# Kernel tuning notes

Hardware: AMD Instinct MI355X
Metric: run time of the kernel (lower is better)

## Reference

```python
import jax, jax.numpy as jnp
import numpy as np

B, C, H, W = 2, 256, 64, 64
NUM_HEADS = 8


def setup_inputs() -> dict:
    key = jax.random.key(0)
    k1, k2, k3 = jax.random.split(key, 3)
    x = jax.random.normal(k1, (B, C, H, W), dtype=jnp.float32)
    # 1x1 convs, bias=False -> plain [out_ch, in_ch] matrices
    w_qkv = jax.random.normal(k2, (3 * C, C), dtype=jnp.float32) * (1.0 / np.sqrt(C))
    w_proj = jax.random.normal(k3, (C, C), dtype=jnp.float32) * (1.0 / np.sqrt(C))
    return {"x": x, "w_qkv": w_qkv, "w_proj": w_proj}


def reference(x, w_qkv, w_proj):
    b, c, h, w = x.shape
    hd = NUM_HEADS
    d = c // hd  # head dim
    n = h * w    # number of tokens

    # 1x1 conv == channel matmul: [3C, C] x [B, C, H, W] -> [B, 3C, H, W]
    qkv = jnp.einsum('oc,bchw->bohw', w_qkv, x)
    q, k, v = jnp.split(qkv, 3, axis=1)

    def reshape(t):
        return t.reshape(b, hd, d, n)  # [B, h, d, N]

    q, k, v = map(reshape, (q, k, v))

    # scores[b,h,i,j] = sum_d q[b,h,d,i] * k[b,h,d,j] / sqrt(d)
    scores = jnp.einsum('bhdi,bhdj->bhij', q, k) / jnp.sqrt(jnp.asarray(d, x.dtype))
    attn = jax.nn.softmax(scores, axis=-1)

    # out[b,h,d,i] = sum_j attn[b,h,i,j] * v[b,h,d,j]
    out = jnp.einsum('bhij,bhdj->bhdi', attn, v)
    out = out.reshape(b, c, h, w)

    return jnp.einsum('oc,bchw->bohw', w_proj, out) + x
```

## Files before the change

### kernel.cpp

```cpp
#include <hip/hip_runtime.h>
#include <hip/hip_bf16.h>

#define NB  2
#define CC  256
#define NHD 8
#define HD  32
#define NT  4096

typedef __bf16 bf16x8 __attribute__((ext_vector_type(8)));
typedef bf16x8 bf16x8_ma __attribute__((may_alias));
typedef __bf16 bf16x4 __attribute__((ext_vector_type(4)));
typedef bf16x4 bf16x4_ma __attribute__((may_alias));
typedef float  f32x4  __attribute__((ext_vector_type(4)));
typedef float  f32x16 __attribute__((ext_vector_type(16)));
typedef unsigned int u32x4 __attribute__((ext_vector_type(4)));

static __device__ __forceinline__ f32x4 zero4() {
    f32x4 z = {0.f, 0.f, 0.f, 0.f}; return z;
}
static __device__ __forceinline__ f32x16 zero16() {
    f32x16 z = {0.f,0.f,0.f,0.f,0.f,0.f,0.f,0.f,
                0.f,0.f,0.f,0.f,0.f,0.f,0.f,0.f};
    return z;
}

#define QSCALE 0.25505392421795654f

#define CVT_PK(dst, lo, hi_) \
    asm("v_cvt_pk_bf16_f32 %0, %1, %2" : "=v"(dst) : "v"(lo), "v"(hi_))
#define PLSWAP(x, y) \
    asm("v_permlane32_swap_b32 %0, %1" : "+v"(x), "+v"(y))


__global__ __launch_bounds__(256) void convw_k(const float* __restrict__ s1,
                                               __bf16* __restrict__ d1, int n1,
                                               const float* __restrict__ s2,
                                               __bf16* __restrict__ d2, int n2) {
    const int i = blockIdx.x * 256 + threadIdx.x;
    if (i < n1) d1[i] = (__bf16)s1[i];
    else if (i - n1 < n2) d2[i - n1] = (__bf16)s2[i - n1];
}

__global__ __launch_bounds__(256) void transpose_k(const float* __restrict__ x,
                                                   __bf16* __restrict__ xt) {
    __shared__ __bf16 T[64][65];
    const int tid = threadIdx.x;
    const int n0 = blockIdx.x * 64, c0 = blockIdx.y * 64, b = blockIdx.z;

#pragma unroll
    for (int rep = 0; rep < 16; ++rep) {
        const int e = rep * 256 + tid;
        const int cl = e >> 6, nl = e & 63;
        T[nl][cl] = (__bf16)x[((size_t)(b * CC + c0 + cl)) * NT + n0 + nl];
    }
    __syncthreads();
#pragma unroll
    for (int rep = 0; rep < 16; ++rep) {
        const int e = rep * 256 + tid;
        const int nl = e >> 6, cl = e & 63;
        xt[((size_t)(b * NT + n0 + nl)) * CC + c0 + cl] = T[nl][cl];
    }
}

__global__ __launch_bounds__(256) void qkv_k(const __bf16* __restrict__ wqkv,
                                             const __bf16* __restrict__ xt,
                                             __bf16* __restrict__ qt,
                                             __bf16* __restrict__ kt,
                                             __bf16* __restrict__ vv) {
    __shared__ __align__(16) __bf16 BF[4][8][512];

    const int lane = threadIdx.x & 63, wv = threadIdx.x >> 6;
    const int g = lane >> 4, c16 = lane & 15;
    const int b    = blockIdx.z;
    const int o0   = blockIdx.y * 64 + wv * 16;
    const int tok0 = blockIdx.x * 64;

    const __bf16* bsrc = xt + ((size_t)(b * NT + tok0 + wv * 16 + c16)) * CC + g * 8;
#pragma unroll
    for (int kc = 0; kc < 8; ++kc) {
        __builtin_amdgcn_global_load_lds(
            (const __attribute__((address_space(1))) void*)(bsrc + kc * 32),
            (__attribute__((address_space(3))) void*)&BF[wv][kc][0],
            16, 0, 0);
    }

    const __bf16* arow = wqkv + (size_t)(o0 + c16) * CC + g * 8;
    bf16x8 a[8];
#pragma unroll
    for (int kc = 0; kc < 8; ++kc) a[kc] = *(const bf16x8_ma*)(arow + kc * 32);

    __syncthreads();

    f32x4 acc[4];
#pragma unroll
    for (int i = 0; i < 4; ++i) acc[i] = zero4();

#pragma unroll
    for (int kc = 0; kc < 8; ++kc) {
#pragma unroll
        for (int js = 0; js < 4; ++js) {
            bf16x8 bb = *(const bf16x8_ma*)&BF[js][kc][lane * 8];
            acc[js] = __builtin_amdgcn_mfma_f32_16x16x32_bf16(a[kc], bb, acc[js], 0, 0, 0);
        }
    }

    const int reg = o0 >> 8;
    const int oo0 = (o0 & 255) + g * 4;
    const int h   = oo0 >> 5;
    const int dd0 = oo0 & 31;
    const size_t bh = (size_t)(b * NHD + h);

#pragma unroll
    for (int js = 0; js < 4; ++js) {
        const int tok = tok0 + js * 16 + c16;
        if (reg == 0) {
            bf16x4 pk;
#pragma unroll
            for (int r = 0; r < 4; ++r) pk[r] = (__bf16)(acc[js][r] * QSCALE);
            *(bf16x4_ma*)(qt + (bh * NT + tok) * HD + dd0) = pk;
        } else if (reg == 1) {
            bf16x4 pk;
#pragma unroll
            for (int r = 0; r < 4; ++r) pk[r] = (__bf16)acc[js][r];
            *(bf16x4_ma*)(kt + (bh * NT + tok) * HD + dd0) = pk;
        } else {
#pragma unroll
            for (int r = 0; r < 4; ++r)
                vv[(bh * HD + dd0 + r) * NT + tok] = (__bf16)acc[js][r];
        }
    }
}

__global__ __launch_bounds__(256, 2) void attn_k(const __bf16* __restrict__ qt,
                                                 const __bf16* __restrict__ kt,
                                                 const __bf16* __restrict__ vv,
                                                 __bf16* __restrict__ ao) {
    __shared__ __align__(16) __bf16 KF[4][2][2][512];
    __shared__ __align__(16) __bf16 VF[4][2][2][512];

    const int tid  = threadIdx.x;
    const int lane = tid & 63, wv = tid >> 6;
    const int c32 = lane & 31, hi = lane >> 5;
    const int bh = blockIdx.y;
    const int b = bh >> 3, h = bh & 7;
    const int i0q = blockIdx.x * 128 + wv * 32;

    const __bf16* qbase = qt + ((size_t)bh * NT + i0q) * HD;
    const __bf16* kbase = kt + (size_t)bh * NT * HD;
    const __bf16* vbase = vv + (size_t)bh * HD * NT;

    const int stg_js = wv & 1, stg_sl = wv >> 1;

    bf16x8 aq0 = *(const bf16x8_ma*)(qbase + (size_t)c32 * HD + hi * 8);
    bf16x8 aq1 = *(const bf16x8_ma*)(qbase + (size_t)c32 * HD + 16 + hi * 8);

    f32x16 oacc = zero16();
    float rsa[4] = {0.f, 0.f, 0.f, 0.f};

#define STAGE(bf, jb) do {                                                              \
    const __bf16* gk = kbase + (size_t)((jb) + stg_js * 32 + c32) * HD                  \
                             + stg_sl * 16 + hi * 8;                                    \
    __builtin_amdgcn_global_load_lds(                                                   \
        (const __attribute__((address_space(1))) void*)gk,                              \
        (__attribute__((address_space(3))) void*)&KF[bf][stg_js][stg_sl][0],            \
        16, 0, 0);                                                                      \
    const __bf16* gv = vbase + (size_t)c32 * NT + (jb) + stg_js * 32                    \
                             + stg_sl * 16 + hi * 8;                                    \
    __builtin_amdgcn_global_load_lds(                                                   \
        (const __attribute__((address_space(1))) void*)gv,                              \
        (__attribute__((address_space(3))) void*)&VF[bf][stg_js][stg_sl][0],            \
        16, 0, 0);                                                                      \
} while (0)

#define SUBTILE(bf, js) do {                                                            \
    bf16x8 fk0 = *(const bf16x8_ma*)&KF[bf][js][0][lane * 8];                           \
    bf16x8 fk1 = *(const bf16x8_ma*)&KF[bf][js][1][lane * 8];                           \
    bf16x8 fv0 = *(const bf16x8_ma*)&VF[bf][js][0][lane * 8];                           \
    bf16x8 fv1 = *(const bf16x8_ma*)&VF[bf][js][1][lane * 8];                           \
    f32x16 s = __builtin_amdgcn_mfma_f32_32x32x16_bf16(fk0, aq0, zero16(), 0, 0, 0);    \
    s = __builtin_amdgcn_mfma_f32_32x32x16_bf16(fk1, aq1, s, 0, 0, 0);                  \
    float p[16];                                                                        \
    _Pragma("unroll")                                                                   \
    for (int r = 0; r < 16; ++r) {                                                      \
        p[r] = __builtin_amdgcn_exp2f(s[r]);                                            \
        rsa[r & 3] += p[r];                                                             \
    }                                                                                   \
    unsigned pk[8];                                                                     \
    _Pragma("unroll")                                                                   \
    for (int i = 0; i < 8; ++i) CVT_PK(pk[i], p[2 * i], p[2 * i + 1]);                  \
    PLSWAP(pk[0], pk[2]);                                                               \
    PLSWAP(pk[1], pk[3]);                                                               \
    PLSWAP(pk[4], pk[6]);                                                               \
    PLSWAP(pk[5], pk[7]);                                                               \
    u32x4 a0 = {pk[0], pk[1], pk[2], pk[3]};                                            \
    u32x4 a1 = {pk[4], pk[5], pk[6], pk[7]};                                            \
    const bf16x8 ap0 = __builtin_bit_cast(bf16x8, a0);                                  \
    const bf16x8 ap1 = __builtin_bit_cast(bf16x8, a1);                                  \
    oacc = __builtin_amdgcn_mfma_f32_32x32x16_bf16(ap0, fv0, oacc, 0, 0, 0);            \
    oacc = __builtin_amdgcn_mfma_f32_32x32x16_bf16(ap1, fv1, oacc, 0, 0, 0);            \
} while (0)

#define TILE_WAIT(VMC) do {                                                             \
    __builtin_amdgcn_sched_barrier(0);                                                  \
    asm volatile("s_waitcnt vmcnt(" #VMC ")" ::: "memory");                             \
    __builtin_amdgcn_s_barrier();                                                       \
    asm volatile("" ::: "memory");                                                      \
    __builtin_amdgcn_sched_barrier(0);                                                  \
} while (0)

    const int NTILES = NT / 64;

    STAGE(0, 0);
    STAGE(1, 64);
    STAGE(2, 128);
    __builtin_amdgcn_sched_barrier(0);

    int t = 0;
#pragma unroll 1
    for (; t < NTILES - 3; ++t) {
        TILE_WAIT(4);
        STAGE((t + 3) & 3, (t + 3) * 64);
        __builtin_amdgcn_s_setprio(1);
        SUBTILE(t & 3, 0);
        SUBTILE(t & 3, 1);
        __builtin_amdgcn_s_setprio(0);
    }
    TILE_WAIT(4);
    __builtin_amdgcn_s_setprio(1);
    SUBTILE(61 & 3, 0); SUBTILE(61 & 3, 1);
    __builtin_amdgcn_s_setprio(0);
    TILE_WAIT(2);
    __builtin_amdgcn_s_setprio(1);
    SUBTILE(62 & 3, 0); SUBTILE(62 & 3, 1);
    __builtin_amdgcn_s_setprio(0);
    TILE_WAIT(0);
    __builtin_amdgcn_s_setprio(1);
    SUBTILE(63 & 3, 0); SUBTILE(63 & 3, 1);
    __builtin_amdgcn_s_setprio(0);

#undef STAGE
#undef SUBTILE
#undef TILE_WAIT

    float rs = (rsa[0] + rsa[1]) + (rsa[2] + rsa[3]);
    rs += __shfl_xor(rs, 32, 64);

#pragma unroll
    for (int g4 = 0; g4 < 4; ++g4) {
#pragma unroll
        for (int r = 0; r < 4; ++r) {
            const int q = 8 * g4 + 4 * hi + r;
            const float lt = __shfl(rs, q, 64);
            ao[((size_t)(b * NT) + i0q + q) * CC + h * HD + c32] =
                (__bf16)(oacc[4 * g4 + r] / lt);
        }
    }
}

__global__ __launch_bounds__(256) void proj_k(const __bf16* __restrict__ wp,
                                              const __bf16* __restrict__ ao,
                                              const float* __restrict__ x,
                                              float* __restrict__ out) {
    __shared__ __align__(16) __bf16 BF[4][8][512];

    const int lane = threadIdx.x & 63, wv = threadIdx.x >> 6;
    const int g = lane >> 4, c16 = lane & 15;
    const int b    = blockIdx.z;
    const int o0   = blockIdx.y * 64 + wv * 16;
    const int tok0 = blockIdx.x * 64;

    const __bf16* bsrc = ao + ((size_t)(b * NT + tok0 + wv * 16 + c16)) * CC + g * 8;
#pragma unroll
    for (int kc = 0; kc < 8; ++kc) {
        __builtin_amdgcn_global_load_lds(
            (const __attribute__((address_space(1))) void*)(bsrc + kc * 32),
            (__attribute__((address_space(3))) void*)&BF[wv][kc][0],
            16, 0, 0);
    }

    const __bf16* arow = wp + (size_t)(o0 + c16) * CC + g * 8;
    bf16x8 a[8];
#pragma unroll
    for (int kc = 0; kc < 8; ++kc) a[kc] = *(const bf16x8_ma*)(arow + kc * 32);

    __syncthreads();

    f32x4 acc[4];
#pragma unroll
    for (int i = 0; i < 4; ++i) acc[i] = zero4();

#pragma unroll
    for (int kc = 0; kc < 8; ++kc) {
#pragma unroll
        for (int js = 0; js < 4; ++js) {
            bf16x8 bb = *(const bf16x8_ma*)&BF[js][kc][lane * 8];
            acc[js] = __builtin_amdgcn_mfma_f32_16x16x32_bf16(a[kc], bb, acc[js], 0, 0, 0);
        }
    }

#pragma unroll
    for (int js = 0; js < 4; ++js) {
        const int tok = tok0 + js * 16 + c16;
#pragma unroll
        for (int r = 0; r < 4; ++r) {
            const int o = o0 + g * 4 + r;
            const size_t idx = ((size_t)(b * CC + o)) * NT + tok;
            out[idx] = acc[js][r] + x[idx];
        }
    }
}

extern "C" void kernel_launch(void* const* d_in, const int* in_sizes, int n_in,
                              void* d_out, int out_size, void* d_ws, size_t ws_size,
                              hipStream_t stream) {
    const int SX  = NB * CC * NT;
    const int SW3 = 3 * CC * CC;
    const int SW1 = CC * CC;
    const size_t E = (size_t)SX;

    const float* x  = nullptr;
    const float* wq = nullptr;
    const float* wp = nullptr;
    for (int i = 0; i < n_in; ++i) {
        const int sz = in_sizes[i];
        if (sz == SX || sz == 2 * SX || sz == 4 * SX)           x  = (const float*)d_in[i];
        else if (sz == SW3 || sz == 2 * SW3 || sz == 4 * SW3)   wq = (const float*)d_in[i];
        else if (sz == SW1 || sz == 2 * SW1 || sz == 4 * SW1)   wp = (const float*)d_in[i];
    }
    if (!x || !wq || !wp) {
        x  = (const float*)d_in[0];
        wq = (const float*)d_in[1];
        wp = (const float*)d_in[2];
    }

    __bf16* ws  = (__bf16*)d_ws;
    __bf16* wqb = ws;
    __bf16* wpb = wqb + SW3;
    __bf16* xt  = wpb + SW1;
    __bf16* qt  = xt + E;
    __bf16* kt  = qt + E;
    __bf16* vv  = kt + E;
    __bf16* ao  = xt;

    float* out = (float*)d_out;

    convw_k<<<dim3((SW3 + SW1 + 255) / 256), 256, 0, stream>>>(wq, wqb, SW3, wp, wpb, SW1);
    transpose_k<<<dim3(NT / 64, CC / 64, NB), 256, 0, stream>>>(x, xt);
    qkv_k<<<dim3(NT / 64, (3 * CC) / 64, NB), 256, 0, stream>>>(wqb, xt, qt, kt, vv);
    attn_k<<<dim3(NT / 128, NB * NHD), 256, 0, stream>>>(qt, kt, vv, ao);
    proj_k<<<dim3(NT / 64, CC / 64, NB), 256, 0, stream>>>(wpb, ao, x, out);
}
```

Before: 151.7 us.

## Split attention over key segments with combine kernel and double buffering

The attention kernel gains a grid z dimension that splits the key range into two segments whenever the workspace is large enough. Each segment writes unnormalised fp32 partial outputs and row sums, and a new combine kernel adds them and normalises into bf16. The pipeline is also cut from a 4-deep staged ring with setprio to a 2-buffer scheme with a full wait and barrier every tile, and launch bounds are raised to 4 blocks per CU. The intent is more blocks to fill the GPU (only 512 blocks before), paid for with partial-result memory traffic, an extra launch, and weaker load overlap.

```diff
diff --git a/kernel.cpp b/kernel.cpp
--- a/kernel.cpp
+++ b/kernel.cpp
@@ -12,6 +12,7 @@
 typedef __bf16 bf16x4 __attribute__((ext_vector_type(4)));
 typedef bf16x4 bf16x4_ma __attribute__((may_alias));
 typedef float  f32x4  __attribute__((ext_vector_type(4)));
+typedef f32x4  f32x4_ma __attribute__((may_alias));
 typedef float  f32x16 __attribute__((ext_vector_type(16)));
 typedef unsigned int u32x4 __attribute__((ext_vector_type(4)));
 
@@ -131,18 +132,21 @@
     }
 }
 
-__global__ __launch_bounds__(256, 2) void attn_k(const __bf16* __restrict__ qt,
+__global__ __launch_bounds__(256, 4) void attn_k(const __bf16* __restrict__ qt,
                                                  const __bf16* __restrict__ kt,
                                                  const __bf16* __restrict__ vv,
-                                                 __bf16* __restrict__ ao) {
-    __shared__ __align__(16) __bf16 KF[4][2][2][512];
-    __shared__ __align__(16) __bf16 VF[4][2][2][512];
+                                                 __bf16* __restrict__ ao,
+                                                 float* __restrict__ PO,
+                                                 float* __restrict__ PL) {
+    __shared__ __align__(16) __bf16 KF[2][2][2][512];
+    __shared__ __align__(16) __bf16 VF[2][2][2][512];
 
     const int tid  = threadIdx.x;
     const int lane = tid & 63, wv = tid >> 6;
     const int c32 = lane & 31, hi = lane >> 5;
     const int bh = blockIdx.y;
     const int b = bh >> 3, h = bh & 7;
+    const int seg = blockIdx.z, nseg = gridDim.z;
     const int i0q = blockIdx.x * 128 + wv * 32;
 
     const __bf16* qbase = qt + ((size_t)bh * NT + i0q) * HD;
@@ -200,61 +204,75 @@
     oacc = __builtin_amdgcn_mfma_f32_32x32x16_bf16(ap1, fv1, oacc, 0, 0, 0);            \
 } while (0)
 
-#define TILE_WAIT(VMC) do {                                                             \
-    __builtin_amdgcn_sched_barrier(0);                                                  \
-    asm volatile("s_waitcnt vmcnt(" #VMC ")" ::: "memory");                             \
-    __builtin_amdgcn_s_barrier();                                                       \
-    asm volatile("" ::: "memory");                                                      \
-    __builtin_amdgcn_sched_barrier(0);                                                  \
-} while (0)
-
-    const int NTILES = NT / 64;
-
-    STAGE(0, 0);
-    STAGE(1, 64);
-    STAGE(2, 128);
-    __builtin_amdgcn_sched_barrier(0);
-
-    int t = 0;
+    const int ntiles  = (NT / 64) / nseg;
+    const int j_begin = seg * ntiles * 64;
+
+    STAGE(0, j_begin);
+    asm volatile("s_waitcnt vmcnt(0)" ::: "memory");
+    __syncthreads();
+
+    int buf = 0;
 #pragma unroll 1
-    for (; t < NTILES - 3; ++t) {
-        TILE_WAIT(4);
-        STAGE((t + 3) & 3, (t + 3) * 64);
-        __builtin_amdgcn_s_setprio(1);
-        SUBTILE(t & 3, 0);
-        SUBTILE(t & 3, 1);
-        __builtin_amdgcn_s_setprio(0);
-    }
-    TILE_WAIT(4);
-    __builtin_amdgcn_s_setprio(1);
-    SUBTILE(61 & 3, 0); SUBTILE(61 & 3, 1);
-    __builtin_amdgcn_s_setprio(0);
-    TILE_WAIT(2);
-    __builtin_amdgcn_s_setprio(1);
-    SUBTILE(62 & 3, 0); SUBTILE(62 & 3, 1);
-    __builtin_amdgcn_s_setprio(0);
-    TILE_WAIT(0);
-    __builtin_amdgcn_s_setprio(1);
-    SUBTILE(63 & 3, 0); SUBTILE(63 & 3, 1);
-    __builtin_amdgcn_s_setprio(0);
+    for (int t = 0; t < ntiles; ++t) {
+        if (t + 1 < ntiles) STAGE(buf ^ 1, j_begin + (t + 1) * 64);
+        SUBTILE(buf, 0);
+        SUBTILE(buf, 1);
+        asm volatile("s_waitcnt vmcnt(0)" ::: "memory");
+        __syncthreads();
+        buf ^= 1;
+    }
 
 #undef STAGE
 #undef SUBTILE
-#undef TILE_WAIT
 
     float rs = (rsa[0] + rsa[1]) + (rsa[2] + rsa[3]);
     rs += __shfl_xor(rs, 32, 64);
 
-#pragma unroll
-    for (int g4 = 0; g4 < 4; ++g4) {
-#pragma unroll
-        for (int r = 0; r < 4; ++r) {
-            const int q = 8 * g4 + 4 * hi + r;
-            const float lt = __shfl(rs, q, 64);
-            ao[((size_t)(b * NT) + i0q + q) * CC + h * HD + c32] =
-                (__bf16)(oacc[4 * g4 + r] / lt);
-        }
-    }
+    if (nseg == 1) {
+#pragma unroll
+        for (int g4 = 0; g4 < 4; ++g4) {
+#pragma unroll
+            for (int r = 0; r < 4; ++r) {
+                const int q = 8 * g4 + 4 * hi + r;
+                const float lt = __shfl(rs, q, 64);
+                ao[((size_t)(b * NT) + i0q + q) * CC + h * HD + c32] =
+                    (__bf16)(oacc[4 * g4 + r] / lt);
+            }
+        }
+    } else {
+        float* po = PO + (((size_t)seg * NB * NHD + bh) * NT + i0q) * HD;
+#pragma unroll
+        for (int g4 = 0; g4 < 4; ++g4) {
+#pragma unroll
+            for (int r = 0; r < 4; ++r) {
+                const int q = 8 * g4 + 4 * hi + r;
+                po[(size_t)q * HD + c32] = oacc[4 * g4 + r];
+            }
+        }
+        if (hi == 0)
+            PL[((size_t)seg * NB * NHD + bh) * NT + i0q + c32] = rs;
+    }
+}
+
+__global__ __launch_bounds__(256) void comb_k(const float* __restrict__ PO,
+                                              const float* __restrict__ PL,
+                                              __bf16* __restrict__ ao) {
+    const int i = blockIdx.x * 256 + threadIdx.x;
+    const int bh = i >> 15;
+    const int rem = i & 32767;
+    const int n = rem >> 3, g = rem & 7;
+    const int b = bh >> 3, h = bh & 7;
+
+    const size_t o0i = (((size_t)bh) * NT + n) * HD + g * 4;
+    const size_t o1i = o0i + (size_t)(NB * NHD) * NT * HD;
+    f32x4 o0 = *(const f32x4_ma*)&PO[o0i];
+    f32x4 o1 = *(const f32x4_ma*)&PO[o1i];
+    const float l = PL[(size_t)bh * NT + n] + PL[(size_t)(NB * NHD) * NT + (size_t)bh * NT + n];
+
+    bf16x4 pk;
+#pragma unroll
+    for (int r = 0; r < 4; ++r) pk[r] = (__bf16)((o0[r] + o1[r]) / l);
+    *(bf16x4_ma*)&ao[((size_t)(b * NT) + n) * CC + h * HD + g * 4] = pk;
 }
 
 __global__ __launch_bounds__(256) void proj_k(const __bf16* __restrict__ wp,
@@ -342,11 +360,20 @@
     __bf16* vv  = kt + E;
     __bf16* ao  = xt;
 
+    const size_t baseB = (size_t)(SW3 + SW1) * 2 + 4 * E * 2;
+    const size_t poB   = 2ull * NB * NHD * NT * HD * 4;
+    const size_t plB   = 2ull * NB * NHD * NT * 4;
+    const int jseg = (ws_size >= baseB + poB + plB) ? 2 : 1;
+    float* PO = (float*)((char*)d_ws + baseB);
+    float* PL = (float*)((char*)d_ws + baseB + poB);
+
     float* out = (float*)d_out;
 
     convw_k<<<dim3((SW3 + SW1 + 255) / 256), 256, 0, stream>>>(wq, wqb, SW3, wp, wpb, SW1);
     transpose_k<<<dim3(NT / 64, CC / 64, NB), 256, 0, stream>>>(x, xt);
     qkv_k<<<dim3(NT / 64, (3 * CC) / 64, NB), 256, 0, stream>>>(wqb, xt, qt, kt, vv);
-    attn_k<<<dim3(NT / 128, NB * NHD), 256, 0, stream>>>(qt, kt, vv, ao);
+    attn_k<<<dim3(NT / 128, NB * NHD, jseg), 256, 0, stream>>>(qt, kt, vv, ao, PO, PL);
+    if (jseg == 2)
+        comb_k<<<dim3((NB * NHD * NT * (HD / 4)) / 256), 256, 0, stream>>>(PO, PL, ao);
     proj_k<<<dim3(NT / 64, CC / 64, NB), 256, 0, stream>>>(wpb, ao, x, out);
 }
```

After: 142.9 us. 1.06x faster.
